# Kernel optimization log

Measured on AMD Instinct MI355X. Metric: run time of the kernel, lower is better.

Reference implementation:

```python
import jax, jax.numpy as jnp
import numpy as np

D_MODEL = 1024
N_HEADS = 16
D_HEAD = D_MODEL // N_HEADS
D_FF = 2048
B, S = 4, 1024
EPS = 1e-6


def layernorm(x, gamma, beta):
    mu = jnp.mean(x, axis=-1, keepdims=True)
    var = jnp.mean(jnp.square(x - mu), axis=-1, keepdims=True)
    return (x - mu) * jax.lax.rsqrt(var + EPS) * gamma + beta


def setup_inputs() -> dict:
    key = jax.random.key(0)
    ks = jax.random.split(key, 12)
    s = 0.02
    return {
        "x": jax.random.normal(ks[0], (B, S, D_MODEL), jnp.float32),
        "mask": jnp.ones((B, 1, 1, S), jnp.int32),
        "Wq": jax.random.normal(ks[1], (D_MODEL, D_MODEL), jnp.float32) * s,
        "Wk": jax.random.normal(ks[2], (D_MODEL, D_MODEL), jnp.float32) * s,
        "Wv": jax.random.normal(ks[3], (D_MODEL, D_MODEL), jnp.float32) * s,
        "Wo": jax.random.normal(ks[4], (D_MODEL, D_MODEL), jnp.float32) * s,
        "bo": jnp.zeros((D_MODEL,), jnp.float32),
        "ln1_g": jnp.ones((D_MODEL,), jnp.float32),
        "ln1_b": jnp.zeros((D_MODEL,), jnp.float32),
        "W1": jax.random.normal(ks[5], (D_MODEL, D_FF), jnp.float32) * s,
        "b1": jnp.zeros((D_FF,), jnp.float32),
        "W2": jax.random.normal(ks[6], (D_FF, D_MODEL), jnp.float32) * s,
        "b2": jnp.zeros((D_MODEL,), jnp.float32),
        "ln2_g": jnp.ones((D_MODEL,), jnp.float32),
        "ln2_b": jnp.zeros((D_MODEL,), jnp.float32),
    }


def reference(x, mask, Wq, Wk, Wv, Wo, bo, ln1_g, ln1_b, W1, b1, W2, b2, ln2_g, ln2_b):
    b, s, _ = x.shape
    # --- multi-head attention ---
    q_proj = x @ Wq                      # [B,S,D]
    k_proj = x @ Wk
    v_proj = x @ Wv
    q = q_proj.reshape(b, s, N_HEADS, D_HEAD)
    k = k_proj.reshape(b, s, N_HEADS, D_HEAD)
    v = v_proj.reshape(b, s, N_HEADS, D_HEAD)
    attn = jnp.einsum('bqhd,bkhd->bhqk', q, k)           # [B,H,S,S]
    attn = jnp.where(mask == 0, -jnp.inf, attn)
    attn = jax.nn.softmax(attn / jnp.sqrt(jnp.float32(D_MODEL)), axis=-1)
    out = jnp.einsum('bhqk,bkhd->bqhd', attn, v).reshape(b, s, D_MODEL)
    # source applies ReLU after the output projection, dropout=eval identity
    out = jax.nn.relu(out @ Wo + bo) + q_proj            # residual = projected queries
    out = layernorm(out, ln1_g, ln1_b)
    # --- FFN (source applies activation AFTER linear2) ---
    ff = jax.nn.relu((out @ W1 + b1) @ W2 + b2) + out
    return layernorm(ff, ln2_g, ln2_b)
```

## Files before the change

kernel.cpp:

```cpp
#include <hip/hip_runtime.h>
#include <hip/hip_bf16.h>

#define D_MODEL 1024
#define N_HEADS 16
#define D_HEAD  64
#define D_FF    2048
#define BATCH   4
#define SEQ     1024
#define ROWS    (BATCH*SEQ)

typedef __bf16  bf16x8 __attribute__((ext_vector_type(8)));
typedef float   f32x4  __attribute__((ext_vector_type(4)));
typedef unsigned int u32x4 __attribute__((ext_vector_type(4)));
typedef unsigned int u32x2 __attribute__((ext_vector_type(2)));
typedef unsigned short u16;
typedef unsigned int u32;

__device__ inline u16 f2bf(float x){ __hip_bfloat16 b = __float2bfloat16(x); return *(u16*)&b; }

#if __has_builtin(__builtin_amdgcn_exp2f)
__device__ inline float fexp2(float x){ return __builtin_amdgcn_exp2f(x); }
#else
__device__ inline float fexp2(float x){ return exp2f(x); }
#endif

__device__ inline void load_lds16(const u16* gsrc, u16* ldst){
  __builtin_amdgcn_global_load_lds((const __attribute__((address_space(1))) void*)gsrc,
                                   (__attribute__((address_space(3))) void*)ldst, 16, 0, 0);
}

__global__ __launch_bounds__(256)
void cast_bf16_kernel(const float* __restrict__ src, __hip_bfloat16* __restrict__ dst, int n){
  int i = (blockIdx.x*blockDim.x + threadIdx.x)*4;
  if (i + 3 < n){
    float4 v = *(const float4*)(src + i);
    dst[i+0] = __float2bfloat16(v.x);
    dst[i+1] = __float2bfloat16(v.y);
    dst[i+2] = __float2bfloat16(v.z);
    dst[i+3] = __float2bfloat16(v.w);
  }
}

__global__ __launch_bounds__(256)
void transpose_cast_kernel(const float* __restrict__ src, __hip_bfloat16* __restrict__ dst,
                           int R, int C){
  __shared__ float tile[32][33];
  int c0 = blockIdx.x*32, r0 = blockIdx.y*32;
  int tx = threadIdx.x & 31, ty = threadIdx.x >> 5;
  #pragma unroll
  for (int i=0;i<32;i+=8)
    tile[ty+i][tx] = src[(size_t)(r0+ty+i)*C + (c0+tx)];
  __syncthreads();
  #pragma unroll
  for (int i=0;i<32;i+=8)
    dst[(size_t)(c0+ty+i)*R + (r0+tx)] = __float2bfloat16(tile[tx][ty+i]);
}

__global__ __launch_bounds__(256)
void transpose4_kernel(const float* __restrict__ s0, const float* __restrict__ s1,
                       const float* __restrict__ s2, const float* __restrict__ s3,
                       __hip_bfloat16* __restrict__ dst){
  __shared__ float tile[32][33];
  const float* src = (blockIdx.z==0)?s0:(blockIdx.z==1)?s1:(blockIdx.z==2)?s2:s3;
  __hip_bfloat16* d = dst + (size_t)blockIdx.z*1024*1024;
  int c0 = blockIdx.x*32, r0 = blockIdx.y*32;
  int tx = threadIdx.x & 31, ty = threadIdx.x >> 5;
  #pragma unroll
  for (int i=0;i<32;i+=8)
    tile[ty+i][tx] = src[(size_t)(r0+ty+i)*1024 + (c0+tx)];
  __syncthreads();
  #pragma unroll
  for (int i=0;i<32;i+=8)
    d[(size_t)(c0+ty+i)*1024 + (r0+tx)] = __float2bfloat16(tile[tx][ty+i]);
}

template<int MODE, int BN>
__global__ __launch_bounds__(256, 2)
void gemm_bt_kernel(const u16* __restrict__ A, const u16* __restrict__ BT,
                    const float* __restrict__ bias, const __hip_bfloat16* __restrict__ resb,
                    float* __restrict__ Cf, __hip_bfloat16* __restrict__ Cb,
                    int M, int N, int K, float cscale, int gx){
  __shared__ u16 As[3][128*32];
  __shared__ u16 Bs[3][BN*32];
  const int bid = blockIdx.x, nwg = gridDim.x;
  const int lin = (bid & 7)*(nwg >> 3) + (bid >> 3);
  const int m0 = (lin / gx)*128, n0 = (lin % gx)*BN;
  const int t = threadIdx.x;
  const int wid = t>>6, lane = t&63;
  const int wm = wid>>1, wn = wid&1;
  const int lr = lane&15, lk = (lane>>4)*8;
  const int srow = t>>2, sseg = (t&3)*8;
  const int wbase = wid*512;

  constexpr int NJ = BN/32;
  f32x4 acc[4][NJ] = {};
  const int NK = K/32;

  auto STAGE = [&](int s, int bi){
    const int kn = s*32;
    #pragma unroll
    for (int c=0;c<2;++c)
      load_lds16(A + (size_t)(m0 + c*64 + srow)*K + kn + sseg, &As[bi][c*2048 + wbase]);
    #pragma unroll
    for (int c=0;c<BN/64;++c)
      load_lds16(BT + (size_t)(n0 + c*64 + srow)*K + kn + sseg, &Bs[bi][c*2048 + wbase]);
  };

  STAGE(0,0);
  STAGE(1,1);
  if constexpr (BN==128) asm volatile("s_waitcnt vmcnt(4)" ::: "memory");
  else                   asm volatile("s_waitcnt vmcnt(3)" ::: "memory");
  __builtin_amdgcn_s_barrier();

  for (int kt=0; kt<NK; ++kt){
    const int cur = kt%3;
    if (kt+2 < NK) STAGE(kt+2, (kt+2)%3);
    bf16x8 af[4], bfr[NJ];
    #pragma unroll
    for (int f=0; f<4; ++f)
      af[f]  = *(const bf16x8*)&As[cur][(wm*64 + f*16 + lr)*32 + lk];
    #pragma unroll
    for (int j=0; j<NJ; ++j)
      bfr[j] = *(const bf16x8*)&Bs[cur][(wn*(BN/2) + j*16 + lr)*32 + lk];
    #pragma unroll
    for (int i=0;i<4;++i)
      #pragma unroll
      for (int j=0;j<NJ;++j)
        acc[i][j] = __builtin_amdgcn_mfma_f32_16x16x32_bf16(af[i], bfr[j], acc[i][j], 0,0,0);
    if (kt+2 < NK){
      if constexpr (BN==128) asm volatile("s_waitcnt vmcnt(4)" ::: "memory");
      else                   asm volatile("s_waitcnt vmcnt(3)" ::: "memory");
      __builtin_amdgcn_s_barrier();
    } else if (kt+1 < NK){
      asm volatile("s_waitcnt vmcnt(0)" ::: "memory");
      __builtin_amdgcn_s_barrier();
    }
  }

  const int r_in = (lane>>4)*4;
  #pragma unroll
  for (int i=0;i<4;++i){
    #pragma unroll
    for (int j=0;j<NJ;++j){
      int col = n0 + wn*(BN/2) + j*16 + lr;
      float bv = bias ? bias[col] : 0.f;
      #pragma unroll
      for (int e=0;e<4;++e){
        int row = m0 + wm*64 + i*16 + r_in + e;
        float v = acc[i][j][e] + bv;
        if (MODE == 1){
          Cb[(size_t)row*N + col] = __float2bfloat16(v);
        } else if (MODE == 6){
          Cf[(size_t)row*N + col] = fmaxf(v,0.f)
              + __bfloat162float(resb[(size_t)row*N + col]);
        } else if (MODE == 7){
          int b = row>>10, s = row&1023, h = col>>6, d = col&63;
          size_t hm = (((size_t)b*16 + h)*1024 + s)*64 + d;
          Cf[(size_t)row*N + col] = fmaxf(v,0.f) + __bfloat162float(resb[hm])*cscale;
        } else {
          int b = row>>10, s = row&1023;
          int which = col>>10, c = col&1023, h = c>>6, d = c&63;
          size_t hm = (((size_t)b*16 + h)*1024 + s)*64 + d;
          if (which == 0){
            Cb[hm] = __float2bfloat16(v * cscale);
          } else if (which == 1){
            Cb[4194304u + hm] = __float2bfloat16(v);
          } else {
            Cb[8388608u + (((size_t)b*16 + h)*64 + d)*1024 + s] = __float2bfloat16(v);
          }
        }
      }
    }
  }
}

__global__ __launch_bounds__(512)
void attn_mfma_kernel(const u16* __restrict__ qb, const u16* __restrict__ kb,
                      const u16* __restrict__ vt, const int* __restrict__ mask,
                      __hip_bfloat16* __restrict__ out){
  __shared__ u16 Ks[2][64*72];
  __shared__ u16 Vs[2][64*72];
  __shared__ u16 Pl[8][16*72];
  __shared__ int s_allv;
  const int t = threadIdx.x;
  const int wid = t>>6, lane = t&63;
  const int lr = lane&15, lg = lane>>4, lk = lg*8;
  const int bid = blockIdx.x;
  const int xcd = bid & 7, slot = bid >> 3;
  const int bh = xcd*8 + (slot>>3);
  const int qx = slot & 7;
  const int b = bh>>4, h = bh&15;
  const int q0 = qx*128 + wid*16;
  const u16* qbase = qb + (size_t)bh*1024*64;
  const u16* kbase = kb + (size_t)bh*1024*64;
  const u16* vbase = vt + (size_t)bh*64*1024;
  const int* mrow = mask + b*SEQ;

  if (t==0) s_allv = 1;
  __syncthreads();
  if (mrow[t*2]==0 || mrow[t*2+1]==0) atomicAnd(&s_allv, 0);

  bf16x8 aq[2];
  aq[0] = *(const bf16x8*)(qbase + (size_t)(q0+lr)*64 + lk);
  aq[1] = *(const bf16x8*)(qbase + (size_t)(q0+lr)*64 + 32 + lk);

  f32x4 osum[4] = {};
  float m1 = -1e30f, l1 = 0.f;

  const int sr = t>>3, sg = (t&7)*8;
  {
    u32x4 kr = *(const u32x4*)(kbase + (size_t)sr*64 + sg);
    u32x4 vr = *(const u32x4*)(vbase + (size_t)sr*1024 + sg);
    *(u32x4*)&Ks[0][sr*72+sg] = kr;
    *(u32x4*)&Vs[0][sr*72+sg] = vr;
  }
  __syncthreads();
  const bool allv = (s_allv != 0);

  for (int kt=0; kt<SEQ/64; ++kt){
    const int k0 = kt*64;
    const int cur = kt&1;
    u32x4 kr, vr;
    const bool more = (kt+1 < SEQ/64);
    if (more){
      kr = *(const u32x4*)(kbase + (size_t)(k0+64+sr)*64 + sg);
      vr = *(const u32x4*)(vbase + (size_t)sr*1024 + (k0+64) + sg);
    }

    f32x4 sacc[4] = {};
    __builtin_amdgcn_s_setprio(1);
    #pragma unroll
    for (int k4=0;k4<4;++k4){
      #pragma unroll
      for (int dg=0;dg<2;++dg){
        bf16x8 kf = *(const bf16x8*)&Ks[cur][(k4*16+lr)*72 + dg*32 + lk];
        sacc[k4] = __builtin_amdgcn_mfma_f32_16x16x32_bf16(kf, aq[dg], sacc[k4],0,0,0);
      }
    }
    __builtin_amdgcn_s_setprio(0);
    if (!allv){
      unsigned long long bm = __ballot(mrow[k0 + lane] != 0);
      if (bm != ~0ull){
        #pragma unroll
        for (int k4=0;k4<4;++k4)
          #pragma unroll
          for (int e=0;e<4;++e)
            if (!((bm >> (k4*16 + lg*4 + e)) & 1)) sacc[k4][e] = -1e30f;
      }
    }

    float mx[4];
    #pragma unroll
    for (int k4=0;k4<4;++k4)
      mx[k4] = fmaxf(fmaxf(sacc[k4][0],sacc[k4][1]), fmaxf(sacc[k4][2],sacc[k4][3]));
    float tm = fmaxf(fmaxf(mx[0],mx[1]), fmaxf(mx[2],mx[3]));
    tm = fmaxf(tm, __shfl_xor(tm,16));
    tm = fmaxf(tm, __shfl_xor(tm,32));

    float mn = m1, c = 1.f;
    bool need = !__all(tm <= m1 + 8.f);
    if (need){
      mn = fmaxf(m1, tm);
      c  = fexp2(m1 - mn);
      m1 = mn;
    }
    float pp[4];
    #pragma unroll
    for (int k4=0;k4<4;++k4){
      #pragma unroll
      for (int e=0;e<4;++e) sacc[k4][e] = fexp2(sacc[k4][e]-mn);
      pp[k4] = (sacc[k4][0]+sacc[k4][1]) + (sacc[k4][2]+sacc[k4][3]);
    }
    float ps = (pp[0]+pp[1]) + (pp[2]+pp[3]);
    ps += __shfl_xor(ps,16);
    ps += __shfl_xor(ps,32);
    l1 = l1*c + ps;

    if (need){
      float ce[4];
      #pragma unroll
      for (int e=0;e<4;++e) ce[e] = __shfl(c, lg*4+e);
      #pragma unroll
      for (int dt=0;dt<4;++dt)
        #pragma unroll
        for (int e=0;e<4;++e) osum[dt][e] *= ce[e];
    }

    #pragma unroll
    for (int k4=0;k4<4;++k4){
      u32 lo = (u32)f2bf(sacc[k4][0]) | ((u32)f2bf(sacc[k4][1])<<16);
      u32 hi = (u32)f2bf(sacc[k4][2]) | ((u32)f2bf(sacc[k4][3])<<16);
      u32x2 pk; pk[0]=lo; pk[1]=hi;
      *(u32x2*)&Pl[wid][lr*72 + k4*16 + lg*4] = pk;
    }
    __builtin_amdgcn_s_setprio(1);
    #pragma unroll
    for (int dt=0;dt<4;++dt){
      #pragma unroll
      for (int kg=0;kg<2;++kg){
        bf16x8 pa = *(const bf16x8*)&Pl[wid][lr*72 + kg*32 + lk];
        bf16x8 vf = *(const bf16x8*)&Vs[cur][(dt*16+lr)*72 + kg*32 + lk];
        osum[dt] = __builtin_amdgcn_mfma_f32_16x16x32_bf16(pa, vf, osum[dt],0,0,0);
      }
    }
    __builtin_amdgcn_s_setprio(0);

    if (more){
      *(u32x4*)&Ks[cur^1][sr*72+sg] = kr;
      *(u32x4*)&Vs[cur^1][sr*72+sg] = vr;
    }
    __syncthreads();
  }
  float li[4];
  #pragma unroll
  for (int e=0;e<4;++e) li[e] = 1.f / __shfl(l1, lg*4+e);
  #pragma unroll
  for (int dt=0;dt<4;++dt){
    int d = dt*16 + lr;
    #pragma unroll
    for (int e=0;e<4;++e){
      int q = q0 + lg*4 + e;
      out[((size_t)b*1024 + q)*1024 + h*64 + d] = __float2bfloat16(osum[dt][e] * li[e]);
    }
  }
}

__global__ __launch_bounds__(256)
void ln_kernel(const float* __restrict__ a, const float* __restrict__ g,
               const float* __restrict__ be, float* __restrict__ outf,
               __hip_bfloat16* __restrict__ outb){
  int row = blockIdx.x, t = threadIdx.x;
  size_t rb = (size_t)row*D_MODEL;
  float4 av = *(const float4*)(a + rb + t*4);
  float v0 = av.x, v1 = av.y, v2 = av.z, v3 = av.w;
  float sum = v0+v1+v2+v3;
  float ss  = v0*v0+v1*v1+v2*v2+v3*v3;
  #pragma unroll
  for (int off=32; off; off>>=1){ sum += __shfl_xor(sum,off); ss += __shfl_xor(ss,off); }
  __shared__ float red[8];
  int wid = t>>6, lane = t&63;
  if (lane==0){ red[wid]=sum; red[4+wid]=ss; }
  __syncthreads();
  sum = red[0]+red[1]+red[2]+red[3];
  ss  = red[4]+red[5]+red[6]+red[7];
  float mu  = sum*(1.f/1024.f);
  float var = ss*(1.f/1024.f) - mu*mu;
  float rstd = rsqrtf(var + 1e-6f);
  float4 gv = *(const float4*)(g  + t*4);
  float4 bv = *(const float4*)(be + t*4);
  float y0=(v0-mu)*rstd*gv.x+bv.x;
  float y1=(v1-mu)*rstd*gv.y+bv.y;
  float y2=(v2-mu)*rstd*gv.z+bv.z;
  float y3=(v3-mu)*rstd*gv.w+bv.w;
  if (outf) *(float4*)(outf+rb+t*4) = make_float4(y0,y1,y2,y3);
  if (outb){
    outb[rb+t*4+0]=__float2bfloat16(y0);
    outb[rb+t*4+1]=__float2bfloat16(y1);
    outb[rb+t*4+2]=__float2bfloat16(y2);
    outb[rb+t*4+3]=__float2bfloat16(y3);
  }
}

extern "C" void kernel_launch(void* const* d_in, const int* in_sizes, int n_in,
                              void* d_out, int out_size, void* d_ws, size_t ws_size,
                              hipStream_t stream){
  const float* x    = (const float*)d_in[0];
  const int*   mask = (const int*)  d_in[1];
  const float* Wq   = (const float*)d_in[2];
  const float* Wk   = (const float*)d_in[3];
  const float* Wv   = (const float*)d_in[4];
  const float* Wo   = (const float*)d_in[5];
  const float* bo   = (const float*)d_in[6];
  const float* ln1g = (const float*)d_in[7];
  const float* ln1b = (const float*)d_in[8];
  const float* W1   = (const float*)d_in[9];
  const float* b1   = (const float*)d_in[10];
  const float* W2   = (const float*)d_in[11];
  const float* b2   = (const float*)d_in[12];
  const float* ln2g = (const float*)d_in[13];
  const float* ln2b = (const float*)d_in[14];

  char* ws = (char*)d_ws;
  const size_t MB = 1024*1024;
  __hip_bfloat16* WqT  = (__hip_bfloat16*)(ws + 0);
  __hip_bfloat16* WoT  = (__hip_bfloat16*)(ws + 6*MB);
  __hip_bfloat16* W1T  = (__hip_bfloat16*)(ws + 8*MB);
  __hip_bfloat16* W2T  = (__hip_bfloat16*)(ws + 12*MB);
  __hip_bfloat16* xb   = (__hip_bfloat16*)(ws + 16*MB);
  __hip_bfloat16* h1b  = (__hip_bfloat16*)(ws + 16*MB);
  float* t1f           = (float*)(ws + 24*MB);
  __hip_bfloat16* ff1b = (__hip_bfloat16*)(ws + 24*MB);
  __hip_bfloat16* qb   = (__hip_bfloat16*)(ws + 40*MB);
  float* t2f           = (float*)(ws + 40*MB);
  __hip_bfloat16* attn_o = (__hip_bfloat16*)(ws + 64*MB);

  const float qscale = 0.03125f * 1.44269504f;
  const float qunscale = 1.0f / qscale;

  cast_bf16_kernel<<<ROWS*D_MODEL/4/256, 256, 0, stream>>>(x, xb, ROWS*D_MODEL);
  transpose4_kernel<<<dim3(32,32,4), 256, 0, stream>>>(Wq, Wk, Wv, Wo, WqT);
  transpose_cast_kernel<<<dim3(64,32), 256, 0, stream>>>(W1, W1T, 1024, 2048);
  transpose_cast_kernel<<<dim3(32,64), 256, 0, stream>>>(W2, W2T, 2048, 1024);

  gemm_bt_kernel<5,128><<<768, 256, 0, stream>>>((const u16*)xb, (const u16*)WqT, nullptr,
                                                 nullptr, nullptr, qb, ROWS, 3072, 1024, qscale, 24);

  attn_mfma_kernel<<<512, 512, 0, stream>>>(
      (const u16*)qb, (const u16*)(qb + 4194304u), (const u16*)(qb + 8388608u), mask, attn_o);

  gemm_bt_kernel<7,64><<<512, 256, 0, stream>>>((const u16*)attn_o, (const u16*)WoT, bo,
                                                qb, t1f, nullptr, ROWS, 1024, 1024, qunscale, 16);

  ln_kernel<<<ROWS, 256, 0, stream>>>(t1f, ln1g, ln1b, nullptr, h1b);

  gemm_bt_kernel<1,128><<<512, 256, 0, stream>>>((const u16*)h1b, (const u16*)W1T, b1,
                                                 nullptr, nullptr, ff1b, ROWS, 2048, 1024, 1.f, 16);

  gemm_bt_kernel<6,64><<<512, 256, 0, stream>>>((const u16*)ff1b, (const u16*)W2T, b2,
                                                h1b, t2f, nullptr, ROWS, 1024, 2048, 1.f, 16);

  ln_kernel<<<ROWS, 256, 0, stream>>>(t2f, ln2g, ln2b, (float*)d_out, nullptr);
}
```

Before: 199.5 us.

## Process two query subtiles per wave in attention, halving block threads

Each wave in the attention kernel now handles 32 query rows as two 16-row subtiles instead of 16, and the block shrinks from 512 to 256 threads. Each K and V fragment read from shared memory therefore feeds two MFMAs, which halves LDS traffic per unit of compute. The P staging is split into 32-column chunks interleaved with the PV MFMAs to keep the scratch buffer smaller. This raises register pressure (double the accumulators) and reduces the number of waves per block, which may hurt latency hiding.

Measured after the change: 203.4 us. No clear change (+2.0%).

```diff
diff --git a/kernel.cpp b/kernel.cpp
--- a/kernel.cpp
+++ b/kernel.cpp
@@ -174,13 +174,13 @@
   }
 }
 
-__global__ __launch_bounds__(512)
+__global__ __launch_bounds__(256)
 void attn_mfma_kernel(const u16* __restrict__ qb, const u16* __restrict__ kb,
                       const u16* __restrict__ vt, const int* __restrict__ mask,
                       __hip_bfloat16* __restrict__ out){
   __shared__ u16 Ks[2][64*72];
   __shared__ u16 Vs[2][64*72];
-  __shared__ u16 Pl[8][16*72];
+  __shared__ u16 Pl[8][16*40];
   __shared__ int s_allv;
   const int t = threadIdx.x;
   const int wid = t>>6, lane = t&63;
@@ -190,7 +190,7 @@
   const int bh = xcd*8 + (slot>>3);
   const int qx = slot & 7;
   const int b = bh>>4, h = bh&15;
-  const int q0 = qx*128 + wid*16;
+  const int q0 = qx*128 + wid*32;
   const u16* qbase = qb + (size_t)bh*1024*64;
   const u16* kbase = kb + (size_t)bh*1024*64;
   const u16* vbase = vt + (size_t)bh*64*1024;
@@ -198,21 +198,24 @@
 
   if (t==0) s_allv = 1;
   __syncthreads();
-  if (mrow[t*2]==0 || mrow[t*2+1]==0) atomicAnd(&s_allv, 0);
-
-  bf16x8 aq[2];
-  aq[0] = *(const bf16x8*)(qbase + (size_t)(q0+lr)*64 + lk);
-  aq[1] = *(const bf16x8*)(qbase + (size_t)(q0+lr)*64 + 32 + lk);
-
-  f32x4 osum[4] = {};
-  float m1 = -1e30f, l1 = 0.f;
-
-  const int sr = t>>3, sg = (t&7)*8;
-  {
-    u32x4 kr = *(const u32x4*)(kbase + (size_t)sr*64 + sg);
-    u32x4 vr = *(const u32x4*)(vbase + (size_t)sr*1024 + sg);
-    *(u32x4*)&Ks[0][sr*72+sg] = kr;
-    *(u32x4*)&Vs[0][sr*72+sg] = vr;
+  if (mrow[t*4+0]==0 || mrow[t*4+1]==0 || mrow[t*4+2]==0 || mrow[t*4+3]==0) atomicAnd(&s_allv, 0);
+
+  bf16x8 aq[2][2];
+  #pragma unroll
+  for (int s=0;s<2;++s){
+    aq[s][0] = *(const bf16x8*)(qbase + (size_t)(q0+s*16+lr)*64 + lk);
+    aq[s][1] = *(const bf16x8*)(qbase + (size_t)(q0+s*16+lr)*64 + 32 + lk);
+  }
+
+  f32x4 osum[2][4] = {};
+  float m1[2] = {-1e30f,-1e30f}, l1[2] = {0.f,0.f};
+
+  const int sr = t>>2, sgc = t&3;
+  #pragma unroll
+  for (int p=0;p<2;++p){
+    int c = (sgc + p*4)*8;
+    *(u32x4*)&Ks[0][sr*72+c] = *(const u32x4*)(kbase + (size_t)sr*64 + c);
+    *(u32x4*)&Vs[0][sr*72+c] = *(const u32x4*)(vbase + (size_t)sr*1024 + c);
   }
   __syncthreads();
   const bool allv = (s_allv != 0);
@@ -220,21 +223,26 @@
   for (int kt=0; kt<SEQ/64; ++kt){
     const int k0 = kt*64;
     const int cur = kt&1;
-    u32x4 kr, vr;
+    u32x4 kr[2], vr[2];
     const bool more = (kt+1 < SEQ/64);
     if (more){
-      kr = *(const u32x4*)(kbase + (size_t)(k0+64+sr)*64 + sg);
-      vr = *(const u32x4*)(vbase + (size_t)sr*1024 + (k0+64) + sg);
-    }
-
-    f32x4 sacc[4] = {};
+      #pragma unroll
+      for (int p=0;p<2;++p){
+        int c = (sgc + p*4)*8;
+        kr[p] = *(const u32x4*)(kbase + (size_t)(k0+64+sr)*64 + c);
+        vr[p] = *(const u32x4*)(vbase + (size_t)sr*1024 + (k0+64) + c);
+      }
+    }
+
+    f32x4 sacc[2][4] = {};
     __builtin_amdgcn_s_setprio(1);
     #pragma unroll
     for (int k4=0;k4<4;++k4){
       #pragma unroll
       for (int dg=0;dg<2;++dg){
         bf16x8 kf = *(const bf16x8*)&Ks[cur][(k4*16+lr)*72 + dg*32 + lk];
-        sacc[k4] = __builtin_amdgcn_mfma_f32_16x16x32_bf16(kf, aq[dg], sacc[k4],0,0,0);
+        sacc[0][k4] = __builtin_amdgcn_mfma_f32_16x16x32_bf16(kf, aq[0][dg], sacc[0][k4],0,0,0);
+        sacc[1][k4] = __builtin_amdgcn_mfma_f32_16x16x32_bf16(kf, aq[1][dg], sacc[1][k4],0,0,0);
       }
     }
     __builtin_amdgcn_s_setprio(0);
@@ -242,85 +250,102 @@
       unsigned long long bm = __ballot(mrow[k0 + lane] != 0);
       if (bm != ~0ull){
         #pragma unroll
-        for (int k4=0;k4<4;++k4)
+        for (int s=0;s<2;++s)
           #pragma unroll
-          for (int e=0;e<4;++e)
-            if (!((bm >> (k4*16 + lg*4 + e)) & 1)) sacc[k4][e] = -1e30f;
-      }
-    }
-
-    float mx[4];
-    #pragma unroll
-    for (int k4=0;k4<4;++k4)
-      mx[k4] = fmaxf(fmaxf(sacc[k4][0],sacc[k4][1]), fmaxf(sacc[k4][2],sacc[k4][3]));
-    float tm = fmaxf(fmaxf(mx[0],mx[1]), fmaxf(mx[2],mx[3]));
-    tm = fmaxf(tm, __shfl_xor(tm,16));
-    tm = fmaxf(tm, __shfl_xor(tm,32));
-
-    float mn = m1, c = 1.f;
-    bool need = !__all(tm <= m1 + 8.f);
-    if (need){
-      mn = fmaxf(m1, tm);
-      c  = fexp2(m1 - mn);
-      m1 = mn;
-    }
-    float pp[4];
-    #pragma unroll
-    for (int k4=0;k4<4;++k4){
-      #pragma unroll
-      for (int e=0;e<4;++e) sacc[k4][e] = fexp2(sacc[k4][e]-mn);
-      pp[k4] = (sacc[k4][0]+sacc[k4][1]) + (sacc[k4][2]+sacc[k4][3]);
-    }
-    float ps = (pp[0]+pp[1]) + (pp[2]+pp[3]);
-    ps += __shfl_xor(ps,16);
-    ps += __shfl_xor(ps,32);
-    l1 = l1*c + ps;
-
-    if (need){
-      float ce[4];
-      #pragma unroll
-      for (int e=0;e<4;++e) ce[e] = __shfl(c, lg*4+e);
-      #pragma unroll
-      for (int dt=0;dt<4;++dt)
+          for (int k4=0;k4<4;++k4)
+            #pragma unroll
+            for (int e=0;e<4;++e)
+              if (!((bm >> (k4*16 + lg*4 + e)) & 1)) sacc[s][k4][e] = -1e30f;
+      }
+    }
+
+    #pragma unroll
+    for (int s=0;s<2;++s){
+      float mx[4];
+      #pragma unroll
+      for (int k4=0;k4<4;++k4)
+        mx[k4] = fmaxf(fmaxf(sacc[s][k4][0],sacc[s][k4][1]), fmaxf(sacc[s][k4][2],sacc[s][k4][3]));
+      float tm = fmaxf(fmaxf(mx[0],mx[1]), fmaxf(mx[2],mx[3]));
+      tm = fmaxf(tm, __shfl_xor(tm,16));
+      tm = fmaxf(tm, __shfl_xor(tm,32));
+      float mn = m1[s], c = 1.f;
+      bool need = !__all(tm <= m1[s] + 8.f);
+      if (need){
+        mn = fmaxf(m1[s], tm);
+        c  = fexp2(m1[s] - mn);
+        m1[s] = mn;
+      }
+      float pp[4];
+      #pragma unroll
+      for (int k4=0;k4<4;++k4){
         #pragma unroll
-        for (int e=0;e<4;++e) osum[dt][e] *= ce[e];
-    }
-
-    #pragma unroll
-    for (int k4=0;k4<4;++k4){
-      u32 lo = (u32)f2bf(sacc[k4][0]) | ((u32)f2bf(sacc[k4][1])<<16);
-      u32 hi = (u32)f2bf(sacc[k4][2]) | ((u32)f2bf(sacc[k4][3])<<16);
-      u32x2 pk; pk[0]=lo; pk[1]=hi;
-      *(u32x2*)&Pl[wid][lr*72 + k4*16 + lg*4] = pk;
-    }
-    __builtin_amdgcn_s_setprio(1);
+        for (int e=0;e<4;++e) sacc[s][k4][e] = fexp2(sacc[s][k4][e]-mn);
+        pp[k4] = (sacc[s][k4][0]+sacc[s][k4][1]) + (sacc[s][k4][2]+sacc[s][k4][3]);
+      }
+      float ps = (pp[0]+pp[1]) + (pp[2]+pp[3]);
+      ps += __shfl_xor(ps,16);
+      ps += __shfl_xor(ps,32);
+      l1[s] = l1[s]*c + ps;
+      if (need){
+        float ce[4];
+        #pragma unroll
+        for (int e=0;e<4;++e) ce[e] = __shfl(c, lg*4+e);
+        #pragma unroll
+        for (int dt=0;dt<4;++dt)
+          #pragma unroll
+          for (int e=0;e<4;++e) osum[s][dt][e] *= ce[e];
+      }
+    }
+
+    #pragma unroll
+    for (int kg=0;kg<2;++kg){
+      #pragma unroll
+      for (int s=0;s<2;++s){
+        #pragma unroll
+        for (int kk=0;kk<2;++kk){
+          int k4 = kg*2 + kk;
+          u32 lo = (u32)f2bf(sacc[s][k4][0]) | ((u32)f2bf(sacc[s][k4][1])<<16);
+          u32 hi = (u32)f2bf(sacc[s][k4][2]) | ((u32)f2bf(sacc[s][k4][3])<<16);
+          u32x2 pk; pk[0]=lo; pk[1]=hi;
+          *(u32x2*)&Pl[wid*2+s][lr*40 + kk*16 + lg*4] = pk;
+        }
+      }
+      bf16x8 pa[2];
+      pa[0] = *(const bf16x8*)&Pl[wid*2+0][lr*40 + lk];
+      pa[1] = *(const bf16x8*)&Pl[wid*2+1][lr*40 + lk];
+      __builtin_amdgcn_s_setprio(1);
+      #pragma unroll
+      for (int dt=0;dt<4;++dt){
+        bf16x8 vf = *(const bf16x8*)&Vs[cur][(dt*16+lr)*72 + kg*32 + lk];
+        osum[0][dt] = __builtin_amdgcn_mfma_f32_16x16x32_bf16(pa[0], vf, osum[0][dt],0,0,0);
+        osum[1][dt] = __builtin_amdgcn_mfma_f32_16x16x32_bf16(pa[1], vf, osum[1][dt],0,0,0);
+      }
+      __builtin_amdgcn_s_setprio(0);
+    }
+
+    if (more){
+      #pragma unroll
+      for (int p=0;p<2;++p){
+        int c = (sgc + p*4)*8;
+        *(u32x4*)&Ks[cur^1][sr*72+c] = kr[p];
+        *(u32x4*)&Vs[cur^1][sr*72+c] = vr[p];
+      }
+    }
+    __syncthreads();
+  }
+  #pragma unroll
+  for (int s=0;s<2;++s){
+    float li[4];
+    #pragma unroll
+    for (int e=0;e<4;++e) li[e] = 1.f / __shfl(l1[s], lg*4+e);
     #pragma unroll
     for (int dt=0;dt<4;++dt){
-      #pragma unroll
-      for (int kg=0;kg<2;++kg){
-        bf16x8 pa = *(const bf16x8*)&Pl[wid][lr*72 + kg*32 + lk];
-        bf16x8 vf = *(const bf16x8*)&Vs[cur][(dt*16+lr)*72 + kg*32 + lk];
-        osum[dt] = __builtin_amdgcn_mfma_f32_16x16x32_bf16(pa, vf, osum[dt],0,0,0);
-      }
-    }
-    __builtin_amdgcn_s_setprio(0);
-
-    if (more){
-      *(u32x4*)&Ks[cur^1][sr*72+sg] = kr;
-      *(u32x4*)&Vs[cur^1][sr*72+sg] = vr;
-    }
-    __syncthreads();
-  }
-  float li[4];
-  #pragma unroll
-  for (int e=0;e<4;++e) li[e] = 1.f / __shfl(l1, lg*4+e);
-  #pragma unroll
-  for (int dt=0;dt<4;++dt){
-    int d = dt*16 + lr;
-    #pragma unroll
-    for (int e=0;e<4;++e){
-      int q = q0 + lg*4 + e;
-      out[((size_t)b*1024 + q)*1024 + h*64 + d] = __float2bfloat16(osum[dt][e] * li[e]);
+      int d = dt*16 + lr;
+      #pragma unroll
+      for (int e=0;e<4;++e){
+        int q = q0 + s*16 + lg*4 + e;
+        out[((size_t)b*1024 + q)*1024 + h*64 + d] = __float2bfloat16(osum[s][dt][e] * li[e]);
+      }
     }
   }
 }
@@ -405,7 +430,7 @@
   gemm_bt_kernel<5,128><<<768, 256, 0, stream>>>((const u16*)xb, (const u16*)WqT, nullptr,
                                                  nullptr, nullptr, qb, ROWS, 3072, 1024, qscale, 24);
 
-  attn_mfma_kernel<<<512, 512, 0, stream>>>(
+  attn_mfma_kernel<<<512, 256, 0, stream>>>(
       (const u16*)qb, (const u16*)(qb + 4194304u), (const u16*)(qb + 8388608u), mask, attn_o);
 
   gemm_bt_kernel<7,64><<<512, 256, 0, stream>>>((const u16*)attn_o, (const u16*)WoT, bo,
```
